# Optimization experiments

Hardware: AMD Instinct MI355X
Metric: run time of the kernel (lower is better)

The kernel has to match this reference:

```python
import jax, jax.numpy as jnp
import numpy as np
from jax import lax

B, N, M = 4, 16384, 512
RADIUS2 = 4.0        # radius=2 (hard-coded in forward), compare squared distances
BALL_K = 64          # k=64 hard-coded in forward
KNN_K = 9            # opt.node_knn_k_1
SIGMA_LB = 0.001     # opt.loss_sigma_lower_bound

_DIMS = [("conv1", 6, 64), ("conv2", 64, 64), ("conv3", 64, 64),
         ("conv4", 128, 128), ("conv5", 128, 128),
         ("knnb1", 131, 256), ("knnb2", 256, 256), ("knnb3", 256, 256),
         ("knna1", 512, 512), ("knna2", 512, 512),
         ("mlp1", 640, 512), ("mlp2", 512, 256)]


def setup_inputs() -> dict:
    key = jax.random.key(0)
    ks = jax.random.split(key, 6)
    inp = {
        "x": jax.random.normal(ks[0], (B, 3, N), jnp.float32),
        "sn": jax.random.normal(ks[1], (B, 3, N), jnp.float32),
        "node": jax.random.normal(ks[2], (B, 3, M), jnp.float32),
    }
    for i, (name, cin, cout) in enumerate(_DIMS):
        k = jax.random.fold_in(ks[3], i)
        inp[name + "_w"] = jax.random.normal(k, (cout, cin), jnp.float32) * np.float32(1.0 / np.sqrt(cin))
        inp[name + "_b"] = jnp.zeros((cout,), jnp.float32)
    inp["mlp3_w"] = jax.random.normal(ks[4], (4, 256), jnp.float32) * np.float32(1e-4)  # .normal_(0, 0.0001)
    inp["mlp3_b"] = jnp.zeros((4,), jnp.float32)
    return inp


def _conv(f, w, b, act=True):
    # 1x1 conv over (B,C,M) or (B,C,M,K): channel matmul + bias (+relu)
    y = jnp.einsum('oc,bc...->bo...', w, f) + b.reshape((1, -1) + (1,) * (f.ndim - 2))
    return jax.nn.relu(y) if act else y


def _sqdist(a, b):
    # a: (B,3,Ma), b: (B,3,Nb) -> (B,Ma,Nb) squared euclidean distances
    aa = jnp.sum(a * a, axis=1)
    bb = jnp.sum(b * b, axis=1)
    ab = jnp.einsum('bcm,bcn->bmn', a, b)
    return aa[:, :, None] + bb[:, None, :] - 2.0 * ab


def _gather(feat, idx):
    # feat: (B,C,Nb), idx: (B,Mq,K) -> (B,C,Mq,K)
    Bq, C, _ = feat.shape
    _, Mq, K = idx.shape
    flat = jnp.broadcast_to(idx.reshape(Bq, 1, Mq * K), (Bq, C, Mq * K))
    return jnp.take_along_axis(feat, flat, axis=2).reshape(Bq, C, Mq, K)


def _ball_query(sqd, radius2, k):
    # first k point indices (in original order) with dist<radius, padded by the first hit
    n = sqd.shape[2]
    mask = sqd < radius2
    keyi = jnp.where(mask, jnp.arange(n, dtype=jnp.int32)[None, None, :], jnp.int32(n))
    _, idx = lax.top_k(-keyi, k)  # k smallest keys == first k in-ball indices
    count = jnp.sum(mask, axis=2, keepdims=True)
    return jnp.where(jnp.arange(k)[None, None, :] < count, idx, idx[:, :, :1])


def reference(x, sn, node,
              conv1_w, conv1_b, conv2_w, conv2_b, conv3_w, conv3_b,
              conv4_w, conv4_b, conv5_w, conv5_b,
              knnb1_w, knnb1_b, knnb2_w, knnb2_b, knnb3_w, knnb3_b,
              knna1_w, knna1_b, knna2_w, knna2_b,
              mlp1_w, mlp1_b, mlp2_w, mlp2_b, mlp3_w, mlp3_b):
    x_aug = jnp.concatenate([x, sn], axis=1)                      # (B,6,N)
    idx = _ball_query(_sqdist(node, x), RADIUS2, BALL_K)          # (B,M,64)
    xb = _gather(x_aug, idx)                                      # (B,6,M,64)
    xb = jnp.concatenate([xb[:, :3] - node[:, :, :, None], xb[:, 3:]], axis=1)
    f = _conv(_conv(_conv(xb, conv1_w, conv1_b), conv2_w, conv2_b), conv3_w, conv3_b)
    fmax = jnp.max(f, axis=3, keepdims=True)
    f = jnp.concatenate([f, jnp.broadcast_to(fmax, f.shape)], axis=1)
    f = _conv(_conv(f, conv4_w, conv4_b), conv5_w, conv5_b)
    feat1 = jnp.max(f, axis=3)                                    # (B,128,M)

    # GeneralKNNFusionModule: query=node, database=node, x=feat1, K=KNN_K
    _, knn_idx = lax.top_k(-_sqdist(node, node), KNN_K)           # (B,M,K) nearest nodes
    coords = _gather(node, knn_idx) - node[:, :, :, None]         # (B,3,M,K)
    g = jnp.concatenate([coords, _gather(feat1, knn_idx)], axis=1)  # (B,131,M,K)
    g = _conv(_conv(_conv(g, knnb1_w, knnb1_b), knnb2_w, knnb2_b), knnb3_w, knnb3_b)
    gmax = jnp.max(g, axis=3, keepdims=True)
    g = jnp.concatenate([g, jnp.broadcast_to(gmax, g.shape)], axis=1)
    g = _conv(_conv(g, knna1_w, knna1_b), knna2_w, knna2_b)
    feat2 = jnp.max(g, axis=3)                                    # (B,512,M)

    h = jnp.concatenate([feat1, feat2], axis=1)                   # (B,640,M)
    h = _conv(_conv(h, mlp1_w, mlp1_b), mlp2_w, mlp2_b)
    ksig = _conv(h, mlp3_w, mlp3_b, act=False)                    # (B,4,M)
    keypoints = ksig[:, :3] + node
    sigmas = jax.nn.softplus(ksig[:, 3]) + SIGMA_LB
    return node, keypoints, sigmas
```

## Files before the change

kernel.cpp:

```cpp
#include <hip/hip_runtime.h>

typedef unsigned short u16;
typedef unsigned int u32;
typedef __bf16 bf16x8 __attribute__((ext_vector_type(8)));
typedef float floatx4 __attribute__((ext_vector_type(4)));
typedef unsigned short u16x8 __attribute__((ext_vector_type(8)));
typedef unsigned int u32x4 __attribute__((ext_vector_type(4)));

static constexpr int B_ = 4;
static constexpr int N_ = 16384;
static constexpr int M_ = 512;

__device__ __forceinline__ u16 f2bf(float f) {
    u32 u = __float_as_uint(f);
    u32 r = (u + 0x7fffu + ((u >> 16) & 1u)) >> 16;
    return (u16)r;
}
__device__ __forceinline__ float bf2f(u16 x) {
    return __uint_as_float(((u32)x) << 16);
}
__device__ __forceinline__ u32 pack2(float a, float b) {
    return (u32)f2bf(a) | ((u32)f2bf(b) << 16);
}

struct WConvArgs { const float* src[12]; };

__global__ __launch_bounds__(256) void prep_kernel(
    const float* __restrict__ x, const float* __restrict__ node,
    int* __restrict__ idx, int* __restrict__ knn,
    WConvArgs wa, u16* __restrict__ Wbf) {
    int bid = blockIdx.x;
    int tid = threadIdx.x, wave = tid >> 6, lane = tid & 63;

    if (bid < 2048) {
        int bm = bid;
        int b = bm >> 9, m = bm & 511;
        __shared__ int sidx[4][64];
        __shared__ int scnt[4];
        const float* xb = x + (size_t)b * 3 * N_;
        float nx = node[((size_t)b * 3 + 0) * M_ + m];
        float ny = node[((size_t)b * 3 + 1) * M_ + m];
        float nz = node[((size_t)b * 3 + 2) * M_ + m];
        float aa = nx * nx + ny * ny + nz * nz;
        int cnt = 0;
        int base = wave * 4096;
        for (int n0 = base; n0 < base + 4096; n0 += 256) {
            float px[4], py[4], pz[4];
#pragma unroll
            for (int i = 0; i < 4; ++i) {
                int n = n0 + i * 64 + lane;
                px[i] = xb[n]; py[i] = xb[N_ + n]; pz[i] = xb[2 * N_ + n];
            }
#pragma unroll
            for (int i = 0; i < 4; ++i) {
                float bb = px[i] * px[i] + py[i] * py[i] + pz[i] * pz[i];
                float d = aa + bb - 2.0f * (nx * px[i] + ny * py[i] + nz * pz[i]);
                bool inb = d < 4.0f;
                unsigned long long mask = __ballot(inb);
                if (inb && cnt < 64) {
                    int pos = cnt + __popcll(mask & ((1ull << lane) - 1ull));
                    if (pos < 64) sidx[wave][pos] = n0 + i * 64 + lane;
                }
                cnt += __popcll(mask);
            }
            if (cnt >= 64) break;
        }
        if (lane == 0) scnt[wave] = cnt;
        __syncthreads();
        if (tid < 64) {
            int total = scnt[0] + scnt[1] + scnt[2] + scnt[3];
            int v = 0;
            if (total > 0) {
                int lim = total < 64 ? total : 64;
                int slot = tid < lim ? tid : 0;
                int w = 0, pre = 0;
                while (w < 3 && slot >= pre + scnt[w]) { pre += scnt[w]; ++w; }
                v = sidx[w][slot - pre];
            }
            idx[(size_t)bm * 64 + tid] = v;
        }
    } else if (bid < 2560) {
        int bm = (bid - 2048) * 4 + wave;
        int b = bm >> 9, m = bm & 511;
        const float* nb = node + (size_t)b * 3 * M_;
        float nx = nb[m], ny = nb[M_ + m], nz = nb[2 * M_ + m];
        float aa = nx * nx + ny * ny + nz * nz;
        float dist[8];
        int didx[8];
#pragma unroll
        for (int i = 0; i < 8; ++i) {
            int n = lane + i * 64;
            float px = nb[n], py = nb[M_ + n], pz = nb[2 * M_ + n];
            float bb = px * px + py * py + pz * pz;
            float ab = nx * px + ny * py + nz * pz;
            dist[i] = aa + bb - 2.0f * ab;
            didx[i] = n;
        }
        for (int r = 0; r < 9; ++r) {
            float bv = dist[0]; int bi = didx[0]; int bslot = 0;
#pragma unroll
            for (int i = 1; i < 8; ++i) {
                if (dist[i] < bv || (dist[i] == bv && didx[i] < bi)) {
                    bv = dist[i]; bi = didx[i]; bslot = i;
                }
            }
            float rv = bv; int ri = bi;
            for (int off = 32; off > 0; off >>= 1) {
                float ov = __shfl_down(rv, off);
                int   oi = __shfl_down(ri, off);
                if (ov < rv || (ov == rv && oi < ri)) { rv = ov; ri = oi; }
            }
            ri = __shfl(ri, 0);
            if (lane == 0) knn[(size_t)bm * 9 + r] = ri;
            if (bi == ri) dist[bslot] = 3.0e38f;
        }
    } else {
        const int CI[12] = {6, 64, 64, 128, 128, 131, 256, 256, 512, 512, 640, 512};
        const int KP[12] = {32, 64, 64, 128, 128, 160, 256, 256, 512, 512, 640, 512};
        const int OFF[13] = {0, 2048, 6144, 10240, 26624, 43008, 83968, 149504,
                             215040, 477184, 739328, 1067008, 1198080};
        int e = (bid - 2560) * 256 + tid;
        int w = 0;
        while (e >= OFF[w + 1]) ++w;
        int local = e - OFF[w];
        int kp = KP[w];
        int co = local / kp, k = local - co * kp;
        float v = 0.0f;
        if (w == 5) {
            if (k < 3) v = wa.src[5][(size_t)co * 131 + k];
            else if (k >= 8 && k < 136) v = wa.src[5][(size_t)co * 131 + (k - 5)];
        } else if (k < CI[w]) {
            v = wa.src[w][(size_t)co * CI[w] + k];
        }
        Wbf[e] = f2bf(v);
    }
}

static constexpr int RS = 136;

__device__ __forceinline__ bf16x8 ldsA(const u16* act, int rf, int l15, int quad, int ks) {
    return *(const bf16x8*)(act + (rf * 16 + l15) * RS + ks * 32 + quad * 8);
}
__device__ __forceinline__ bf16x8 ldW(const u16* W, int ks, int l15, int quad, int kstride) {
    return *(const bf16x8*)(W + (size_t)l15 * kstride + ks * 32 + quad * 8);
}

__global__ __launch_bounds__(256, 3) void fused_stage1_kernel(
    const float* __restrict__ x, const float* __restrict__ sn,
    const float* __restrict__ node, const int* __restrict__ idx,
    const u16* __restrict__ Wbf,
    const float* __restrict__ b1, const float* __restrict__ b2,
    const float* __restrict__ b3, const float* __restrict__ b4,
    const float* __restrict__ b5, u16* __restrict__ h) {
    __shared__ __align__(16) u16 act[128 * RS];
    __shared__ __align__(16) u16 mv[2][64];
    int blk = blockIdx.x;
    int bm0 = blk * 2;
    int tid = threadIdx.x, wave = tid >> 6, lane = tid & 63;
    int quad = lane >> 4, l15 = lane & 15;

    {
        int row = tid & 127, grp = tid >> 7;
        int bm = bm0 + (row >> 6);
        int b = bm >> 9, m = bm & 511;
        int j = idx[(size_t)bm * 64 + (row & 63)];
        const float* xb = x + (size_t)b * 3 * N_;
        const float* sb = sn + (size_t)b * 3 * N_;
        u16* r = act + row * RS;
        if (grp == 0) {
            float c0 = xb[j]          - node[((size_t)b * 3 + 0) * M_ + m];
            float c1 = xb[N_ + j]     - node[((size_t)b * 3 + 1) * M_ + m];
            float c2 = xb[2 * N_ + j] - node[((size_t)b * 3 + 2) * M_ + m];
            *(u32*)(r)     = pack2(c0, c1);
            *(u32*)(r + 2) = pack2(c2, sb[j]);
        } else {
            *(u32*)(r + 4) = pack2(sb[N_ + j], sb[2 * N_ + j]);
            *(u32*)(r + 6) = 0u;
            u32x4* z = (u32x4*)(r + 8);
            z[0] = (u32x4){0u, 0u, 0u, 0u};
            z[1] = (u32x4){0u, 0u, 0u, 0u};
            z[2] = (u32x4){0u, 0u, 0u, 0u};
        }
    }
    __syncthreads();

    {
        const u16* Wp = Wbf + (size_t)(wave * 16) * 32;
        bf16x8 bw = ldW(Wp, 0, l15, quad, 32);
        floatx4 c[8];
#pragma unroll
        for (int rf = 0; rf < 8; ++rf) {
            bf16x8 a = ldsA(act, rf, l15, quad, 0);
            c[rf] = __builtin_amdgcn_mfma_f32_16x16x32_bf16(a, bw, (floatx4){0.f,0.f,0.f,0.f}, 0, 0, 0);
        }
        float bias = b1[wave * 16 + l15];
        __syncthreads();
#pragma unroll
        for (int rf = 0; rf < 8; ++rf)
#pragma unroll
            for (int r = 0; r < 4; ++r)
                act[(rf * 16 + quad * 4 + r) * RS + wave * 16 + l15] = f2bf(fmaxf(c[rf][r] + bias, 0.0f));
        __syncthreads();
    }

    const int WOFF23[2] = {2048, 6144};
    const float* bp23[2] = {b2, b3};
#pragma unroll 1
    for (int cv = 0; cv < 2; ++cv) {
        const u16* Wp = Wbf + WOFF23[cv] + (size_t)(wave * 16) * 64;
        bf16x8 bw0 = ldW(Wp, 0, l15, quad, 64);
        bf16x8 bw1 = ldW(Wp, 1, l15, quad, 64);
        floatx4 c[8] = {};
#pragma unroll
        for (int ks = 0; ks < 2; ++ks)
#pragma unroll
            for (int rf = 0; rf < 8; ++rf) {
                bf16x8 a = ldsA(act, rf, l15, quad, ks);
                c[rf] = __builtin_amdgcn_mfma_f32_16x16x32_bf16(a, ks ? bw1 : bw0, c[rf], 0, 0, 0);
            }
        float bias = bp23[cv][wave * 16 + l15];
        float mxA = 0.0f, mxB = 0.0f;
#pragma unroll
        for (int rf = 0; rf < 8; ++rf)
#pragma unroll
            for (int r = 0; r < 4; ++r) {
                float v = fmaxf(c[rf][r] + bias, 0.0f);
                if (rf < 4) mxA = fmaxf(mxA, v); else mxB = fmaxf(mxB, v);
            }
        __syncthreads();
#pragma unroll
        for (int rf = 0; rf < 8; ++rf)
#pragma unroll
            for (int r = 0; r < 4; ++r)
                act[(rf * 16 + quad * 4 + r) * RS + wave * 16 + l15] = f2bf(fmaxf(c[rf][r] + bias, 0.0f));
        if (cv == 1) {
            mxA = fmaxf(mxA, __shfl_xor(mxA, 16));
            mxA = fmaxf(mxA, __shfl_xor(mxA, 32));
            mxB = fmaxf(mxB, __shfl_xor(mxB, 16));
            mxB = fmaxf(mxB, __shfl_xor(mxB, 32));
            if (quad == 0) {
                mv[0][wave * 16 + l15] = f2bf(mxA);
                mv[1][wave * 16 + l15] = f2bf(mxB);
            }
        }
        __syncthreads();
    }

    {
        const u16* Wp = Wbf + 10240 + (size_t)(wave * 32) * 128;
        bf16x8 bw[2][4];
#pragma unroll
        for (int cf = 0; cf < 2; ++cf)
#pragma unroll
            for (int ks = 0; ks < 4; ++ks)
                bw[cf][ks] = ldW(Wp + (size_t)cf * 16 * 128, ks, l15, quad, 128);
        floatx4 c[8][2] = {};
#pragma unroll
        for (int ks = 0; ks < 4; ++ks)
#pragma unroll
            for (int rf = 0; rf < 8; ++rf) {
                bf16x8 a = (ks < 2) ? ldsA(act, rf, l15, quad, ks)
                                    : *(const bf16x8*)(&mv[rf >> 2][(ks - 2) * 32 + quad * 8]);
#pragma unroll
                for (int cf = 0; cf < 2; ++cf)
                    c[rf][cf] = __builtin_amdgcn_mfma_f32_16x16x32_bf16(a, bw[cf][ks], c[rf][cf], 0, 0, 0);
            }
        float bias[2];
#pragma unroll
        for (int cf = 0; cf < 2; ++cf) bias[cf] = b4[wave * 32 + cf * 16 + l15];
        __syncthreads();
#pragma unroll
        for (int rf = 0; rf < 8; ++rf)
#pragma unroll
            for (int cf = 0; cf < 2; ++cf)
#pragma unroll
                for (int r = 0; r < 4; ++r)
                    act[(rf * 16 + quad * 4 + r) * RS + wave * 32 + cf * 16 + l15] =
                        f2bf(fmaxf(c[rf][cf][r] + bias[cf], 0.0f));
        __syncthreads();
    }

    {
        const u16* Wp = Wbf + 26624 + (size_t)(wave * 32) * 128;
        bf16x8 bw[2][4];
#pragma unroll
        for (int cf = 0; cf < 2; ++cf)
#pragma unroll
            for (int ks = 0; ks < 4; ++ks)
                bw[cf][ks] = ldW(Wp + (size_t)cf * 16 * 128, ks, l15, quad, 128);
        floatx4 c[8][2] = {};
#pragma unroll
        for (int ks = 0; ks < 4; ++ks)
#pragma unroll
            for (int rf = 0; rf < 8; ++rf) {
                bf16x8 a = ldsA(act, rf, l15, quad, ks);
#pragma unroll
                for (int cf = 0; cf < 2; ++cf)
                    c[rf][cf] = __builtin_amdgcn_mfma_f32_16x16x32_bf16(a, bw[cf][ks], c[rf][cf], 0, 0, 0);
            }
#pragma unroll
        for (int cf = 0; cf < 2; ++cf) {
            float bias = b5[wave * 32 + cf * 16 + l15];
            float mxA = 0.0f, mxB = 0.0f;
#pragma unroll
            for (int rf = 0; rf < 8; ++rf)
#pragma unroll
                for (int r = 0; r < 4; ++r) {
                    float v = fmaxf(c[rf][cf][r] + bias, 0.0f);
                    if (rf < 4) mxA = fmaxf(mxA, v); else mxB = fmaxf(mxB, v);
                }
            mxA = fmaxf(mxA, __shfl_xor(mxA, 16));
            mxA = fmaxf(mxA, __shfl_xor(mxA, 32));
            mxB = fmaxf(mxB, __shfl_xor(mxB, 16));
            mxB = fmaxf(mxB, __shfl_xor(mxB, 32));
            if (quad == 0) {
                h[(size_t)bm0 * 640 + wave * 32 + cf * 16 + l15] = f2bf(mxA);
                h[(size_t)(bm0 + 1) * 640 + wave * 32 + cf * 16 + l15] = f2bf(mxB);
            }
        }
    }
}

template <int KS, int CF, int RF, int RSx>
__device__ __forceinline__ void conv_inplace(u16* act, const u16* __restrict__ W0, int KP,
                                             const float* __restrict__ bias, int cb,
                                             int l15, int quad) {
    floatx4 acc[RF][CF];
#pragma unroll
    for (int rf = 0; rf < RF; ++rf)
#pragma unroll
        for (int cf = 0; cf < CF; ++cf) acc[rf][cf] = (floatx4){0.f, 0.f, 0.f, 0.f};

    bf16x8 bw[4][CF];
#pragma unroll
    for (int p = 0; p < 3; ++p)
        if (p < KS)
#pragma unroll
            for (int cf = 0; cf < CF; ++cf)
                bw[p][cf] = *(const bf16x8*)(W0 + (size_t)(cb + cf * 16 + l15) * KP +
                                             p * 32 + quad * 8);

#pragma unroll
    for (int ks = 0; ks < KS; ++ks) {
        if (ks + 3 < KS) {
#pragma unroll
            for (int cf = 0; cf < CF; ++cf)
                bw[(ks + 3) & 3][cf] = *(const bf16x8*)(W0 + (size_t)(cb + cf * 16 + l15) * KP +
                                                        (ks + 3) * 32 + quad * 8);
        }
#pragma unroll
        for (int rf = 0; rf < RF; ++rf) {
            bf16x8 a = *(const bf16x8*)(act + (rf * 16 + l15) * RSx + ks * 32 + quad * 8);
#pragma unroll
            for (int cf = 0; cf < CF; ++cf)
                acc[rf][cf] = __builtin_amdgcn_mfma_f32_16x16x32_bf16(a, bw[ks & 3][cf], acc[rf][cf], 0, 0, 0);
        }
    }
    __syncthreads();
#pragma unroll
    for (int cf = 0; cf < CF; ++cf) {
        float bs = bias[cb + cf * 16 + l15];
#pragma unroll
        for (int rf = 0; rf < RF; ++rf)
#pragma unroll
            for (int r = 0; r < 4; ++r)
                act[(rf * 16 + quad * 4 + r) * RSx + cb + cf * 16 + l15] =
                    f2bf(fmaxf(acc[rf][cf][r] + bs, 0.0f));
    }
    __syncthreads();
}

static constexpr int RS2 = 520;

__global__ __launch_bounds__(512, 2) void fused_stage2_kernel(
    const float* __restrict__ node, u16* __restrict__ h, const int* __restrict__ knn,
    const u16* __restrict__ Wbf,
    const float* __restrict__ bb1, const float* __restrict__ bb2,
    const float* __restrict__ bb3, const float* __restrict__ ba1,
    const float* __restrict__ ba2) {
    __shared__ __align__(16) u16 act[80 * RS2];
    int blk = blockIdx.x;
    int node0 = blk * 8;
    int b = node0 >> 9;
    int tid = threadIdx.x, wave = tid >> 6, lane = tid & 63;
    int quad = lane >> 4, l15 = lane & 15;
    (void)lane;

    for (int e = tid; e < 80 * 20; e += 512)
        *(u16x8*)(act + (e / 20) * RS2 + (e % 20) * 8) = (u16x8){0,0,0,0,0,0,0,0};
    __syncthreads();
    for (int e = tid; e < 72 * 3; e += 512) {
        int r = e / 3, c = e - r * 3;
        int nodei = node0 + r / 9;
        int j = knn[(size_t)nodei * 9 + (r % 9)];
        float v = node[((size_t)b * 3 + c) * M_ + j] - node[((size_t)b * 3 + c) * M_ + (nodei & 511)];
        act[r * RS2 + c] = f2bf(v);
    }
    for (int e = tid; e < 72 * 16; e += 512) {
        int r = e >> 4, s = e & 15;
        int nodei = node0 + r / 9;
        int j = knn[(size_t)nodei * 9 + (r % 9)];
        *(u16x8*)(act + r * RS2 + 8 + s * 8) =
            *(const u16x8*)(h + (size_t)(b * 512 + j) * 640 + s * 8);
    }
    __syncthreads();

    conv_inplace<5, 2, 5, RS2>(act, Wbf + 43008, 160, bb1, wave * 32, l15, quad);
    conv_inplace<8, 2, 5, RS2>(act, Wbf + 83968, 256, bb2, wave * 32, l15, quad);
    conv_inplace<8, 2, 5, RS2>(act, Wbf + 149504, 256, bb3, wave * 32, l15, quad);

    for (int e = tid; e < 8 * 32; e += 512) {
        int li = e >> 5, s = e & 31;
        int r0 = li * 9;
        float mx[8];
#pragma unroll
        for (int i = 0; i < 8; ++i) mx[i] = -3.0e38f;
#pragma unroll
        for (int kk = 0; kk < 9; ++kk) {
            u16x8 v = *(const u16x8*)(act + (r0 + kk) * RS2 + s * 8);
#pragma unroll
            for (int i = 0; i < 8; ++i) mx[i] = fmaxf(mx[i], bf2f(v[i]));
        }
        u16x8 o;
#pragma unroll
        for (int i = 0; i < 8; ++i) o[i] = f2bf(mx[i]);
#pragma unroll
        for (int kk = 0; kk < 9; ++kk)
            *(u16x8*)(act + (r0 + kk) * RS2 + 256 + s * 8) = o;
    }
    __syncthreads();

    conv_inplace<16, 4, 5, RS2>(act, Wbf + 215040, 512, ba1, wave * 64, l15, quad);
    conv_inplace<16, 4, 5, RS2>(act, Wbf + 477184, 512, ba2, wave * 64, l15, quad);

    for (int e = tid; e < 8 * 64; e += 512) {
        int li = e >> 6, s = e & 63;
        int r0 = li * 9;
        float mx[8];
#pragma unroll
        for (int i = 0; i < 8; ++i) mx[i] = -3.0e38f;
#pragma unroll
        for (int kk = 0; kk < 9; ++kk) {
            u16x8 v = *(const u16x8*)(act + (r0 + kk) * RS2 + s * 8);
#pragma unroll
            for (int i = 0; i < 8; ++i) mx[i] = fmaxf(mx[i], bf2f(v[i]));
        }
        u16x8 o;
#pragma unroll
        for (int i = 0; i < 8; ++i) o[i] = f2bf(mx[i]);
        *(u16x8*)(h + (size_t)(node0 + li) * 640 + 128 + s * 8) = o;
    }
}

static constexpr int RS3 = 648;

__global__ __launch_bounds__(512, 2) void fused_stage3_kernel(
    const float* __restrict__ node, const u16* __restrict__ h,
    const u16* __restrict__ Wbf,
    const float* __restrict__ bm1, const float* __restrict__ bm2,
    const float* __restrict__ w3, const float* __restrict__ b3,
    float* __restrict__ out) {
    __shared__ __align__(16) u16 act[16 * RS3];
    int blk = blockIdx.x;
    int node0 = blk * 8;
    int tid = threadIdx.x, lane = tid & 63, wave = tid >> 6;
    int quad = lane >> 4, l15 = lane & 15;

    for (int e = tid; e < 16 * 80; e += 512) {
        int r = e / 80, seg = e - r * 80;
        u16x8 v = (r < 8) ? *(const u16x8*)(h + (size_t)(node0 + r) * 640 + seg * 8)
                          : (u16x8){0,0,0,0,0,0,0,0};
        *(u16x8*)(act + r * RS3 + seg * 8) = v;
    }
    __syncthreads();

    conv_inplace<20, 4, 1, RS3>(act, Wbf + 739328, 640, bm1, wave * 64, l15, quad);
    conv_inplace<16, 2, 1, RS3>(act, Wbf + 1067008, 512, bm2, wave * 32, l15, quad);

    if (tid < 32) {
        int li = tid >> 2, oc = tid & 3;
        const u16* row = act + li * RS3;
        const float* wrow = w3 + oc * 256;
        float a = 0.0f;
        for (int c = 0; c < 256; c += 4) {
            a += bf2f(row[c]) * wrow[c];
            a += bf2f(row[c + 1]) * wrow[c + 1];
            a += bf2f(row[c + 2]) * wrow[c + 2];
            a += bf2f(row[c + 3]) * wrow[c + 3];
        }
        a += b3[oc];
        int nodei = node0 + li;
        int b = nodei >> 9, m = nodei & 511;
        if (oc < 3) {
            float nv = node[((size_t)b * 3 + oc) * M_ + m];
            out[((size_t)b * 3 + oc) * M_ + m] = nv;
            out[6144 + ((size_t)b * 3 + oc) * M_ + m] = nv + a;
        } else {
            out[12288 + nodei] = fmaxf(a, 0.0f) + log1pf(expf(-fabsf(a))) + 0.001f;
        }
    }
}

extern "C" void kernel_launch(void* const* d_in, const int* in_sizes, int n_in,
                              void* d_out, int out_size, void* d_ws, size_t ws_size,
                              hipStream_t stream) {
    (void)in_sizes; (void)n_in; (void)out_size; (void)ws_size;
    const float* x = (const float*)d_in[0];
    const float* sn = (const float*)d_in[1];
    const float* node = (const float*)d_in[2];
    const float* W[13];
    const float* Bs[13];
    for (int i = 0; i < 13; ++i) {
        W[i] = (const float*)d_in[3 + 2 * i];
        Bs[i] = (const float*)d_in[4 + 2 * i];
    }
    float* out = (float*)d_out;

    char* ws = (char*)d_ws;
    int* idx = (int*)(ws + 0);
    int* knn = (int*)(ws + 524288);
    u16* Wbf = (u16*)(ws + 598016);
    u16* h   = (u16*)(ws + 2994176);

    WConvArgs wa;
    for (int w = 0; w < 12; ++w) wa.src[w] = W[w];

    prep_kernel<<<7240, 256, 0, stream>>>(x, node, idx, knn, wa, Wbf);

    fused_stage1_kernel<<<1024, 256, 0, stream>>>(x, sn, node, idx, Wbf,
                                                  Bs[0], Bs[1], Bs[2], Bs[3], Bs[4], h);
    fused_stage2_kernel<<<256, 512, 0, stream>>>(node, h, knn, Wbf,
                                                 Bs[5], Bs[6], Bs[7], Bs[8], Bs[9]);
    fused_stage3_kernel<<<256, 512, 0, stream>>>(node, h, Wbf, Bs[10], Bs[11],
                                                 W[12], Bs[12], out);
}
```

Baseline: 225.1 us.

## Fuse stage2 and stage3 kernels, keeping node features in shared memory

Merges the KNN-fusion stage and the final MLP stage into one kernel. The per-node max-pooled features stay in LDS instead of being written to the global h buffer and read back, and the act buffer is reused with the stage-3 stride layout. Only the first 128 channels of h (stage-1 output) are still loaded from global memory. It also lowers stage1 launch bounds from 3 to 2 blocks per SM, which gives the compiler more registers per thread at the cost of occupancy.

```diff
diff --git a/kernel.cpp b/kernel.cpp
--- a/kernel.cpp
+++ b/kernel.cpp
@@ -145,7 +145,7 @@
     return *(const bf16x8*)(W + (size_t)l15 * kstride + ks * 32 + quad * 8);
 }
 
-__global__ __launch_bounds__(256, 3) void fused_stage1_kernel(
+__global__ __launch_bounds__(256, 2) void fused_stage1_kernel(
     const float* __restrict__ x, const float* __restrict__ sn,
     const float* __restrict__ node, const int* __restrict__ idx,
     const u16* __restrict__ Wbf,
@@ -371,13 +371,17 @@
 }
 
 static constexpr int RS2 = 520;
-
-__global__ __launch_bounds__(512, 2) void fused_stage2_kernel(
-    const float* __restrict__ node, u16* __restrict__ h, const int* __restrict__ knn,
+static constexpr int RS3 = 648;
+
+__global__ __launch_bounds__(512, 2) void fused_stage23_kernel(
+    const float* __restrict__ node, const u16* __restrict__ h, const int* __restrict__ knn,
     const u16* __restrict__ Wbf,
     const float* __restrict__ bb1, const float* __restrict__ bb2,
     const float* __restrict__ bb3, const float* __restrict__ ba1,
-    const float* __restrict__ ba2) {
+    const float* __restrict__ ba2,
+    const float* __restrict__ bm1, const float* __restrict__ bm2,
+    const float* __restrict__ w3, const float* __restrict__ b3,
+    float* __restrict__ out) {
     __shared__ __align__(16) u16 act[80 * RS2];
     int blk = blockIdx.x;
     int node0 = blk * 8;
@@ -433,44 +437,46 @@
     conv_inplace<16, 4, 5, RS2>(act, Wbf + 215040, 512, ba1, wave * 64, l15, quad);
     conv_inplace<16, 4, 5, RS2>(act, Wbf + 477184, 512, ba2, wave * 64, l15, quad);
 
-    for (int e = tid; e < 8 * 64; e += 512) {
-        int li = e >> 6, s = e & 63;
+    float pm[8];
+    {
+        int li = tid >> 6, s = tid & 63;
         int r0 = li * 9;
-        float mx[8];
-#pragma unroll
-        for (int i = 0; i < 8; ++i) mx[i] = -3.0e38f;
+#pragma unroll
+        for (int i = 0; i < 8; ++i) pm[i] = -3.0e38f;
 #pragma unroll
         for (int kk = 0; kk < 9; ++kk) {
             u16x8 v = *(const u16x8*)(act + (r0 + kk) * RS2 + s * 8);
 #pragma unroll
-            for (int i = 0; i < 8; ++i) mx[i] = fmaxf(mx[i], bf2f(v[i]));
-        }
+            for (int i = 0; i < 8; ++i) pm[i] = fmaxf(pm[i], bf2f(v[i]));
+        }
+    }
+    __syncthreads();
+
+    {
+        int li = tid >> 6, s = tid & 63;
         u16x8 o;
 #pragma unroll
-        for (int i = 0; i < 8; ++i) o[i] = f2bf(mx[i]);
-        *(u16x8*)(h + (size_t)(node0 + li) * 640 + 128 + s * 8) = o;
-    }
-}
-
-static constexpr int RS3 = 648;
-
-__global__ __launch_bounds__(512, 2) void fused_stage3_kernel(
-    const float* __restrict__ node, const u16* __restrict__ h,
-    const u16* __restrict__ Wbf,
-    const float* __restrict__ bm1, const float* __restrict__ bm2,
-    const float* __restrict__ w3, const float* __restrict__ b3,
-    float* __restrict__ out) {
-    __shared__ __align__(16) u16 act[16 * RS3];
-    int blk = blockIdx.x;
-    int node0 = blk * 8;
-    int tid = threadIdx.x, lane = tid & 63, wave = tid >> 6;
-    int quad = lane >> 4, l15 = lane & 15;
-
-    for (int e = tid; e < 16 * 80; e += 512) {
-        int r = e / 80, seg = e - r * 80;
-        u16x8 v = (r < 8) ? *(const u16x8*)(h + (size_t)(node0 + r) * 640 + seg * 8)
-                          : (u16x8){0,0,0,0,0,0,0,0};
-        *(u16x8*)(act + r * RS3 + seg * 8) = v;
+        for (int i = 0; i < 8; ++i) o[i] = f2bf(pm[i]);
+        *(u16x8*)(act + li * RS3 + 128 + s * 8) = o;
+    }
+    for (int e = tid; e < 16 * 16 + 8 * 81; e += 512) {
+        if (e < 16 * 16) {
+            int r = 8 + (e >> 4), s = e & 15;
+            *(u16x8*)(act + r * RS3 + s * 8) = (u16x8){0,0,0,0,0,0,0,0};
+        } else {
+            int e2 = e - 256;
+            int r = e2 / 81, s = e2 - r * 81;
+            if (s < 16) {
+                *(u16x8*)(act + r * RS3 + s * 8) =
+                    *(const u16x8*)(h + (size_t)(node0 + r) * 640 + s * 8);
+            } else if (s == 80) {
+                *(u16x8*)(act + r * RS3 + 640) = (u16x8){0,0,0,0,0,0,0,0};
+            }
+        }
+    }
+    for (int e = tid; e < 8 * 65; e += 512) {
+        int r = 8 + e / 65, s = 16 + e % 65;
+        *(u16x8*)(act + r * RS3 + s * 8) = (u16x8){0,0,0,0,0,0,0,0};
     }
     __syncthreads();
 
@@ -490,11 +496,11 @@
         }
         a += b3[oc];
         int nodei = node0 + li;
-        int b = nodei >> 9, m = nodei & 511;
+        int bb = nodei >> 9, m = nodei & 511;
         if (oc < 3) {
-            float nv = node[((size_t)b * 3 + oc) * M_ + m];
-            out[((size_t)b * 3 + oc) * M_ + m] = nv;
-            out[6144 + ((size_t)b * 3 + oc) * M_ + m] = nv + a;
+            float nv = node[((size_t)bb * 3 + oc) * M_ + m];
+            out[((size_t)bb * 3 + oc) * M_ + m] = nv;
+            out[6144 + ((size_t)bb * 3 + oc) * M_ + m] = nv + a;
         } else {
             out[12288 + nodei] = fmaxf(a, 0.0f) + log1pf(expf(-fabsf(a))) + 0.001f;
         }
@@ -529,8 +535,7 @@
 
     fused_stage1_kernel<<<1024, 256, 0, stream>>>(x, sn, node, idx, Wbf,
                                                   Bs[0], Bs[1], Bs[2], Bs[3], Bs[4], h);
-    fused_stage2_kernel<<<256, 512, 0, stream>>>(node, h, knn, Wbf,
-                                                 Bs[5], Bs[6], Bs[7], Bs[8], Bs[9]);
-    fused_stage3_kernel<<<256, 512, 0, stream>>>(node, h, Wbf, Bs[10], Bs[11],
-                                                 W[12], Bs[12], out);
-}
+    fused_stage23_kernel<<<256, 512, 0, stream>>>(node, h, knn, Wbf,
+                                                  Bs[5], Bs[6], Bs[7], Bs[8], Bs[9],
+                                                  Bs[10], Bs[11], W[12], Bs[12], out);
+}
```

Result: no change. 227.0 us (+0.9%).

## Precompute packed float4 points with squared norms for ball query; split prep kernel

Applied to the files above, without the earlier changes.

Adds a pass that packs each point's xyz and squared norm into one float4 buffer, and splits the prep kernel into two launches so the ball query reads one aligned 16-byte load per point instead of three strided loads plus norm arithmetic. The ball query loop now steps 64 points at a time, so it can stop early at a finer granularity, but it no longer issues four loads ahead. Stage1's launch bounds drop the minimum blocks per CU from 3 to 2, which gives the compiler more registers per thread at possible cost to occupancy. It costs an extra kernel launch and an extra 1 MB write and read.

```diff
diff --git a/kernel.cpp b/kernel.cpp
--- a/kernel.cpp
+++ b/kernel.cpp
@@ -25,101 +25,23 @@
 
 struct WConvArgs { const float* src[12]; };
 
-__global__ __launch_bounds__(256) void prep_kernel(
-    const float* __restrict__ x, const float* __restrict__ node,
-    int* __restrict__ idx, int* __restrict__ knn,
-    WConvArgs wa, u16* __restrict__ Wbf) {
+__global__ __launch_bounds__(256) void prep_a_kernel(
+    const float* __restrict__ x, WConvArgs wa,
+    float4* __restrict__ pk, u16* __restrict__ Wbf) {
     int bid = blockIdx.x;
-    int tid = threadIdx.x, wave = tid >> 6, lane = tid & 63;
-
-    if (bid < 2048) {
-        int bm = bid;
-        int b = bm >> 9, m = bm & 511;
-        __shared__ int sidx[4][64];
-        __shared__ int scnt[4];
+    int tid = threadIdx.x;
+    if (bid < 256) {
+        int t = bid * 256 + tid;
+        int b = t >> 14, n = t & (N_ - 1);
         const float* xb = x + (size_t)b * 3 * N_;
-        float nx = node[((size_t)b * 3 + 0) * M_ + m];
-        float ny = node[((size_t)b * 3 + 1) * M_ + m];
-        float nz = node[((size_t)b * 3 + 2) * M_ + m];
-        float aa = nx * nx + ny * ny + nz * nz;
-        int cnt = 0;
-        int base = wave * 4096;
-        for (int n0 = base; n0 < base + 4096; n0 += 256) {
-            float px[4], py[4], pz[4];
-#pragma unroll
-            for (int i = 0; i < 4; ++i) {
-                int n = n0 + i * 64 + lane;
-                px[i] = xb[n]; py[i] = xb[N_ + n]; pz[i] = xb[2 * N_ + n];
-            }
-#pragma unroll
-            for (int i = 0; i < 4; ++i) {
-                float bb = px[i] * px[i] + py[i] * py[i] + pz[i] * pz[i];
-                float d = aa + bb - 2.0f * (nx * px[i] + ny * py[i] + nz * pz[i]);
-                bool inb = d < 4.0f;
-                unsigned long long mask = __ballot(inb);
-                if (inb && cnt < 64) {
-                    int pos = cnt + __popcll(mask & ((1ull << lane) - 1ull));
-                    if (pos < 64) sidx[wave][pos] = n0 + i * 64 + lane;
-                }
-                cnt += __popcll(mask);
-            }
-            if (cnt >= 64) break;
-        }
-        if (lane == 0) scnt[wave] = cnt;
-        __syncthreads();
-        if (tid < 64) {
-            int total = scnt[0] + scnt[1] + scnt[2] + scnt[3];
-            int v = 0;
-            if (total > 0) {
-                int lim = total < 64 ? total : 64;
-                int slot = tid < lim ? tid : 0;
-                int w = 0, pre = 0;
-                while (w < 3 && slot >= pre + scnt[w]) { pre += scnt[w]; ++w; }
-                v = sidx[w][slot - pre];
-            }
-            idx[(size_t)bm * 64 + tid] = v;
-        }
-    } else if (bid < 2560) {
-        int bm = (bid - 2048) * 4 + wave;
-        int b = bm >> 9, m = bm & 511;
-        const float* nb = node + (size_t)b * 3 * M_;
-        float nx = nb[m], ny = nb[M_ + m], nz = nb[2 * M_ + m];
-        float aa = nx * nx + ny * ny + nz * nz;
-        float dist[8];
-        int didx[8];
-#pragma unroll
-        for (int i = 0; i < 8; ++i) {
-            int n = lane + i * 64;
-            float px = nb[n], py = nb[M_ + n], pz = nb[2 * M_ + n];
-            float bb = px * px + py * py + pz * pz;
-            float ab = nx * px + ny * py + nz * pz;
-            dist[i] = aa + bb - 2.0f * ab;
-            didx[i] = n;
-        }
-        for (int r = 0; r < 9; ++r) {
-            float bv = dist[0]; int bi = didx[0]; int bslot = 0;
-#pragma unroll
-            for (int i = 1; i < 8; ++i) {
-                if (dist[i] < bv || (dist[i] == bv && didx[i] < bi)) {
-                    bv = dist[i]; bi = didx[i]; bslot = i;
-                }
-            }
-            float rv = bv; int ri = bi;
-            for (int off = 32; off > 0; off >>= 1) {
-                float ov = __shfl_down(rv, off);
-                int   oi = __shfl_down(ri, off);
-                if (ov < rv || (ov == rv && oi < ri)) { rv = ov; ri = oi; }
-            }
-            ri = __shfl(ri, 0);
-            if (lane == 0) knn[(size_t)bm * 9 + r] = ri;
-            if (bi == ri) dist[bslot] = 3.0e38f;
-        }
+        float px = xb[n], py = xb[N_ + n], pz = xb[2 * N_ + n];
+        pk[t] = make_float4(px, py, pz, px * px + py * py + pz * pz);
     } else {
         const int CI[12] = {6, 64, 64, 128, 128, 131, 256, 256, 512, 512, 640, 512};
         const int KP[12] = {32, 64, 64, 128, 128, 160, 256, 256, 512, 512, 640, 512};
         const int OFF[13] = {0, 2048, 6144, 10240, 26624, 43008, 83968, 149504,
                              215040, 477184, 739328, 1067008, 1198080};
-        int e = (bid - 2560) * 256 + tid;
+        int e = (bid - 256) * 256 + tid;
         int w = 0;
         while (e >= OFF[w + 1]) ++w;
         int local = e - OFF[w];
@@ -136,6 +58,88 @@
     }
 }
 
+__global__ __launch_bounds__(256) void prep_b_kernel(
+    const float4* __restrict__ pk, const float* __restrict__ node,
+    int* __restrict__ idx, int* __restrict__ knn) {
+    int bid = blockIdx.x;
+    int tid = threadIdx.x, wave = tid >> 6, lane = tid & 63;
+
+    if (bid < 2048) {
+        int bm = bid;
+        int b = bm >> 9, m = bm & 511;
+        __shared__ int sidx[4][64];
+        __shared__ int scnt[4];
+        const float4* pb = pk + ((size_t)b << 14);
+        float nx = node[((size_t)b * 3 + 0) * M_ + m];
+        float ny = node[((size_t)b * 3 + 1) * M_ + m];
+        float nz = node[((size_t)b * 3 + 2) * M_ + m];
+        float aa = nx * nx + ny * ny + nz * nz;
+        int cnt = 0;
+        int base = wave * 4096;
+        for (int n0 = base; n0 < base + 4096; n0 += 64) {
+            float4 p = pb[n0 + lane];
+            float d = aa + p.w - 2.0f * (nx * p.x + ny * p.y + nz * p.z);
+            bool inb = d < 4.0f;
+            unsigned long long mask = __ballot(inb);
+            if (inb && cnt < 64) {
+                int pos = cnt + __popcll(mask & ((1ull << lane) - 1ull));
+                if (pos < 64) sidx[wave][pos] = n0 + lane;
+            }
+            cnt += __popcll(mask);
+            if (cnt >= 64) break;
+        }
+        if (lane == 0) scnt[wave] = cnt;
+        __syncthreads();
+        if (tid < 64) {
+            int total = scnt[0] + scnt[1] + scnt[2] + scnt[3];
+            int v = 0;
+            if (total > 0) {
+                int lim = total < 64 ? total : 64;
+                int slot = tid < lim ? tid : 0;
+                int w = 0, pre = 0;
+                while (w < 3 && slot >= pre + scnt[w]) { pre += scnt[w]; ++w; }
+                v = sidx[w][slot - pre];
+            }
+            idx[(size_t)bm * 64 + tid] = v;
+        }
+    } else {
+        int bm = (bid - 2048) * 4 + wave;
+        int b = bm >> 9, m = bm & 511;
+        const float* nb = node + (size_t)b * 3 * M_;
+        float nx = nb[m], ny = nb[M_ + m], nz = nb[2 * M_ + m];
+        float aa = nx * nx + ny * ny + nz * nz;
+        float dist[8];
+        int didx[8];
+#pragma unroll
+        for (int i = 0; i < 8; ++i) {
+            int n = lane + i * 64;
+            float px = nb[n], py = nb[M_ + n], pz = nb[2 * M_ + n];
+            float bb = px * px + py * py + pz * pz;
+            float ab = nx * px + ny * py + nz * pz;
+            dist[i] = aa + bb - 2.0f * ab;
+            didx[i] = n;
+        }
+        for (int r = 0; r < 9; ++r) {
+            float bv = dist[0]; int bi = didx[0]; int bslot = 0;
+#pragma unroll
+            for (int i = 1; i < 8; ++i) {
+                if (dist[i] < bv || (dist[i] == bv && didx[i] < bi)) {
+                    bv = dist[i]; bi = didx[i]; bslot = i;
+                }
+            }
+            float rv = bv; int ri = bi;
+            for (int off = 32; off > 0; off >>= 1) {
+                float ov = __shfl_down(rv, off);
+                int   oi = __shfl_down(ri, off);
+                if (ov < rv || (ov == rv && oi < ri)) { rv = ov; ri = oi; }
+            }
+            ri = __shfl(ri, 0);
+            if (lane == 0) knn[(size_t)bm * 9 + r] = ri;
+            if (bi == ri) dist[bslot] = 3.0e38f;
+        }
+    }
+}
+
 static constexpr int RS = 136;
 
 __device__ __forceinline__ bf16x8 ldsA(const u16* act, int rf, int l15, int quad, int ks) {
@@ -145,7 +149,7 @@
     return *(const bf16x8*)(W + (size_t)l15 * kstride + ks * 32 + quad * 8);
 }
 
-__global__ __launch_bounds__(256, 3) void fused_stage1_kernel(
+__global__ __launch_bounds__(256, 2) void fused_stage1_kernel(
     const float* __restrict__ x, const float* __restrict__ sn,
     const float* __restrict__ node, const int* __restrict__ idx,
     const u16* __restrict__ Wbf,
@@ -521,11 +525,13 @@
     int* knn = (int*)(ws + 524288);
     u16* Wbf = (u16*)(ws + 598016);
     u16* h   = (u16*)(ws + 2994176);
+    float4* pk = (float4*)(ws + 5615616);
 
     WConvArgs wa;
     for (int w = 0; w < 12; ++w) wa.src[w] = W[w];
 
-    prep_kernel<<<7240, 256, 0, stream>>>(x, node, idx, knn, wa, Wbf);
+    prep_a_kernel<<<4936, 256, 0, stream>>>(x, wa, pk, Wbf);
+    prep_b_kernel<<<2560, 256, 0, stream>>>(pk, node, idx, knn);
 
     fused_stage1_kernel<<<1024, 256, 0, stream>>>(x, sn, node, idx, Wbf,
                                                   Bs[0], Bs[1], Bs[2], Bs[3], Bs[4], h);
```

New measurement: 243.6 us. +8.2%, slower.
